# Performance work log

Measured on AMD Instinct MI355X. Metric: run time of the kernel, lower is better.

## Reference

```python
import jax, jax.numpy as jnp
import numpy as np

QUERY_DIM = 1024
KEY_DIM = 1024
NUM_HEADS = 16
HEAD_DIM = QUERY_DIM // NUM_HEADS


def setup_inputs() -> dict:
    key = jax.random.key(0)
    ks = jax.random.split(key, 11)
    B, Sq, Sk = 2, 2048, 2048
    s = 0.02
    return {
        "q": jax.random.normal(ks[0], (B, Sq, QUERY_DIM), jnp.float32),
        "k": jax.random.normal(ks[1], (B, Sk, KEY_DIM), jnp.float32),
        "v": jax.random.normal(ks[2], (B, Sk, KEY_DIM), jnp.float32),
        "Wq": jax.random.normal(ks[3], (QUERY_DIM, QUERY_DIM), jnp.float32) * s,
        "bq": jnp.zeros((QUERY_DIM,), jnp.float32),
        "Wk": jax.random.normal(ks[4], (KEY_DIM, QUERY_DIM), jnp.float32) * s,
        "bk": jnp.zeros((QUERY_DIM,), jnp.float32),
        "Wv": jax.random.normal(ks[5], (KEY_DIM, QUERY_DIM), jnp.float32) * s,
        "bv": jnp.zeros((QUERY_DIM,), jnp.float32),
        "Wo": jax.random.normal(ks[6], (QUERY_DIM, QUERY_DIM), jnp.float32) * s,
        "bo": jnp.zeros((QUERY_DIM,), jnp.float32),
    }


def reference(q, k, v, Wq, bq, Wk, bk, Wv, bv, Wo, bo):
    B, Sq, _ = q.shape
    Sk = k.shape[1]
    scale = HEAD_DIM ** -0.5
    # projections -> [B, H, S, Dh]
    qh = (q @ Wq + bq).reshape(B, Sq, NUM_HEADS, HEAD_DIM).transpose(0, 2, 1, 3)
    kh = (k @ Wk + bk).reshape(B, Sk, NUM_HEADS, HEAD_DIM).transpose(0, 2, 1, 3)
    vh = (v @ Wv + bv).reshape(B, Sk, NUM_HEADS, HEAD_DIM).transpose(0, 2, 1, 3)
    scores = jnp.einsum("bhqd,bhkd->bhqk", qh, kh) * scale
    attn = jax.nn.softmax(scores, axis=-1)
    out = jnp.einsum("bhqk,bhkd->bhqd", attn, vh)
    out = out.transpose(0, 2, 1, 3).reshape(B, Sq, QUERY_DIM)
    return out @ Wo + bo  # dropout is identity at inference
```

## Files before the change

### kernel.cpp

```cpp
#include <hip/hip_runtime.h>
#include <hip/hip_fp16.h>
#include <cstddef>


#define B_   2
#define S_   2048
#define D_   1024
#define H_   16
#define DH_  64

typedef _Float16 half8 __attribute__((ext_vector_type(8)));
typedef _Float16 half4 __attribute__((ext_vector_type(4)));
typedef float floatx4 __attribute__((ext_vector_type(4)));

#define MFMA32(a, b, c) __builtin_amdgcn_mfma_f32_16x16x32_f16((a), (b), (c), 0, 0, 0)
#define MFMA16(a, b, c) __builtin_amdgcn_mfma_f32_16x16x16f16((a), (b), (c), 0, 0, 0)

__global__ __launch_bounds__(256) void cvt3(
    const float* __restrict__ q, const float* __restrict__ k,
    const float* __restrict__ v,
    __half* __restrict__ qf, __half* __restrict__ kf, __half* __restrict__ vf)
{
    const float* srcs[3] = {q, k, v};
    __half* dsts[3] = {qf, kf, vf};
    const int z = blockIdx.y;
    const int i = blockIdx.x * 256 + threadIdx.x;
    const float4* s = (const float4*)srcs[z];
    const float4 a = s[2 * i], b = s[2 * i + 1];
    half8 h;
    h[0] = (_Float16)a.x; h[1] = (_Float16)a.y; h[2] = (_Float16)a.z; h[3] = (_Float16)a.w;
    h[4] = (_Float16)b.x; h[5] = (_Float16)b.y; h[6] = (_Float16)b.z; h[7] = (_Float16)b.w;
    *(half8*)&dsts[z][(size_t)i * 8] = h;
}

__global__ __launch_bounds__(256) void wtrans4(
    const float* __restrict__ Wq, const float* __restrict__ Wk,
    const float* __restrict__ Wv, const float* __restrict__ Wo,
    __half* __restrict__ Wtq, __half* __restrict__ Wtk,
    __half* __restrict__ Wtv, __half* __restrict__ Wto)
{
    __shared__ __align__(16) __half T[64][72];
    const float* Ws[4] = {Wq, Wk, Wv, Wo};
    __half* Wts[4] = {Wtq, Wtk, Wtv, Wto};
    const float* W = Ws[blockIdx.z];
    __half* Wt = Wts[blockIdx.z];
    const int tid = threadIdx.x;
    const int n0 = blockIdx.x * 64, k0 = blockIdx.y * 64;
    #pragma unroll
    for (int p = 0; p < 4; ++p) {
        const int c = tid + p * 256;
        const int kr = c >> 4, nc = (c & 15) * 4;
        const float4 a = *(const float4*)&W[(size_t)(k0 + kr) * D_ + n0 + nc];
        T[nc + 0][kr] = __float2half(a.x);
        T[nc + 1][kr] = __float2half(a.y);
        T[nc + 2][kr] = __float2half(a.z);
        T[nc + 3][kr] = __float2half(a.w);
    }
    __syncthreads();
    #pragma unroll
    for (int p = 0; p < 2; ++p) {
        const int c = tid + p * 256;
        const int nr = c >> 3, kc = (c & 7) * 8;
        *(half8*)&Wt[(size_t)(n0 + nr) * D_ + k0 + kc] = *(const half8*)&T[nr][kc];
    }
}

__device__ __forceinline__ void gemm_core(
    const __half* __restrict__ A, const __half* __restrict__ Bt,
    const float* __restrict__ bias, void* __restrict__ dst,
    const int mode, const float oscale)
{
    __shared__ __align__(16) char gsm[36864];
    __half (*As)[72] = (__half(*)[72])gsm;
    __half (*Bs)[72] = (__half(*)[72])(gsm + 18432);

    const int tid = threadIdx.x;
    const int m0 = blockIdx.y * 128, n0 = blockIdx.x * 128;
    const int lane = tid & 63, wv = tid >> 6;
    const int quad = lane >> 4, lr = lane & 15;
    const int wm0 = (wv >> 1) * 64, wn0 = (wv & 1) * 64;

    floatx4 acc[4][4];
    #pragma unroll
    for (int i = 0; i < 4; ++i)
        #pragma unroll
        for (int j = 0; j < 4; ++j)
            acc[i][j] = (floatx4){0.f, 0.f, 0.f, 0.f};

    half8 pa[4], pb[4];
    #pragma unroll
    for (int p = 0; p < 4; ++p) {
        const int c = tid + p * 256;
        const int row = c >> 3, seg = (c & 7) * 8;
        pa[p] = *(const half8*)&A [(size_t)(m0 + row) * D_ + seg];
        pb[p] = *(const half8*)&Bt[(size_t)(n0 + row) * D_ + seg];
    }

    for (int k0 = 0; k0 < D_; k0 += 64) {
        __syncthreads();
        #pragma unroll
        for (int p = 0; p < 4; ++p) {
            const int c = tid + p * 256;
            const int row = c >> 3, seg = (c & 7) * 8;
            *(half8*)&As[row][seg] = pa[p];
            *(half8*)&Bs[row][seg] = pb[p];
        }
        if (k0 + 64 < D_) {
            #pragma unroll
            for (int p = 0; p < 4; ++p) {
                const int c = tid + p * 256;
                const int row = c >> 3, seg = (c & 7) * 8;
                pa[p] = *(const half8*)&A [(size_t)(m0 + row) * D_ + k0 + 64 + seg];
                pb[p] = *(const half8*)&Bt[(size_t)(n0 + row) * D_ + k0 + 64 + seg];
            }
        }
        __syncthreads();
        #pragma unroll
        for (int ks = 0; ks < 2; ++ks) {
            const int ko = quad * 8 + ks * 32;
            half8 af[4], bf[4];
            #pragma unroll
            for (int i = 0; i < 4; ++i) af[i] = *(const half8*)&As[wm0 + i * 16 + lr][ko];
            #pragma unroll
            for (int j = 0; j < 4; ++j) bf[j] = *(const half8*)&Bs[wn0 + j * 16 + lr][ko];
            #pragma unroll
            for (int i = 0; i < 4; ++i)
                #pragma unroll
                for (int j = 0; j < 4; ++j)
                    acc[i][j] = MFMA32(af[i], bf[j], acc[i][j]);
        }
    }

    if (mode == 1) {
        float* out = (float*)dst;
        #pragma unroll
        for (int i = 0; i < 4; ++i) {
            #pragma unroll
            for (int j = 0; j < 4; ++j) {
                const int col = n0 + wn0 + j * 16 + lr;
                const float bval = bias[col];
                #pragma unroll
                for (int r = 0; r < 4; ++r) {
                    const int m = m0 + wm0 + i * 16 + quad * 4 + r;
                    out[(size_t)m * D_ + col] = acc[i][j][r] + bval;
                }
            }
        }
        return;
    }

    __syncthreads();
    __half (*Ct)[136] = (__half(*)[136])gsm;
    #pragma unroll
    for (int i = 0; i < 4; ++i) {
        #pragma unroll
        for (int j = 0; j < 4; ++j) {
            const int nl = wn0 + j * 16 + lr;
            const float bval = bias[n0 + nl];
            #pragma unroll
            for (int r = 0; r < 4; ++r) {
                const int ml = wm0 + i * 16 + quad * 4 + r;
                const _Float16 hv = (_Float16)((acc[i][j][r] + bval) * oscale);
                if (mode == 0) Ct[ml][nl] = hv;
                else           Ct[nl][ml] = hv;
            }
        }
    }
    __syncthreads();
    __half* oh = (__half*)dst;
    #pragma unroll
    for (int p = 0; p < 8; ++p) {
        const int row = (tid >> 4) + p * 16;
        const int cs  = (tid & 15) * 8;
        const half8 vls = *(const half8*)&Ct[row][cs];
        if (mode == 0) {
            const int m = m0 + row, col = n0 + cs;
            const int b = m >> 11, s = m & (S_ - 1);
            const int h = col >> 6, d = col & 63;
            *(half8*)&oh[(((size_t)(b * H_ + h) * S_ + s) << 6) + d] = vls;
        } else {
            const int col = n0 + row, m = m0 + cs;
            const int b = m >> 11, s = m & (S_ - 1);
            const int h = col >> 6, d = col & 63;
            *(half8*)&oh[((size_t)(b * H_ + h) * DH_ + d) * S_ + s] = vls;
        }
    }
}

__global__ __launch_bounds__(256) void gemm_proj(
    const __half* __restrict__ qf, const __half* __restrict__ kf,
    const __half* __restrict__ vf,
    const __half* __restrict__ Wtq, const __half* __restrict__ Wtk,
    const __half* __restrict__ Wtv,
    const float* __restrict__ bq, const float* __restrict__ bk,
    const float* __restrict__ bv,
    __half* __restrict__ qhf, __half* __restrict__ khf, __half* __restrict__ vht)
{
    const __half* As[3] = {qf, kf, vf};
    const __half* Bts[3] = {Wtq, Wtk, Wtv};
    const float* bs[3] = {bq, bk, bv};
    __half* ds[3] = {qhf, khf, vht};
    const int z = blockIdx.z;
    gemm_core(As[z], Bts[z], bs[z], ds[z], z == 2 ? 2 : 0,
              z == 0 ? 0.1803368801111244f : 1.0f);
}

__global__ __launch_bounds__(256) void gemm_final(
    const __half* __restrict__ attf, const __half* __restrict__ Wto,
    const float* __restrict__ bo, float* __restrict__ out)
{
    gemm_core(attf, Wto, bo, out, 1, 1.0f);
}

__global__ __launch_bounds__(256) void attn_f16(
    const __half* __restrict__ qhf, const __half* __restrict__ khf,
    const __half* __restrict__ vht, __half* __restrict__ attf)
{
    __shared__ __align__(16) char smem[31232];
    __half (*Qs)[72] = (__half(*)[72])smem;
    __half (*Ks)[72] = (__half(*)[72])(smem + 9216);
    __half (*Vs)[72] = (__half(*)[72])(smem + 18432);

    const int tid = threadIdx.x;
    const int lane = tid & 63, wv = tid >> 6;
    const int quad = lane >> 4, lr = lane & 15;
    const int bh = blockIdx.y;
    const int q0 = blockIdx.x * 64;
    const size_t hbase = (size_t)bh * S_ * DH_;

    #pragma unroll
    for (int p = 0; p < 2; ++p) {
        const int c = tid + p * 256;
        const int row = c >> 3, seg = (c & 7) * 8;
        *(half8*)&Qs[row][seg] = *(const half8*)&qhf[hbase + (size_t)(q0 + row) * DH_ + seg];
    }
    __syncthreads();
    half8 qB[4][2];
    #pragma unroll
    for (int qs = 0; qs < 4; ++qs)
        #pragma unroll
        for (int ks = 0; ks < 2; ++ks)
            qB[qs][ks] = *(const half8*)&Qs[qs * 16 + lr][quad * 8 + ks * 32];

    float lp[4] = {0.f, 0.f, 0.f, 0.f};
    floatx4 O[4][4];
    #pragma unroll
    for (int i = 0; i < 4; ++i)
        #pragma unroll
        for (int j = 0; j < 4; ++j)
            O[i][j] = (floatx4){0.f, 0.f, 0.f, 0.f};

    half8 pk[2], pv[2];
    #pragma unroll
    for (int p = 0; p < 2; ++p) {
        const int c = tid + p * 256;
        const int row = c >> 3, seg = (c & 7) * 8;
        pk[p] = *(const half8*)&khf[hbase + (size_t)row * DH_ + seg];
        pv[p] = *(const half8*)&vht[hbase + (size_t)row * S_ + seg];
    }

    for (int kt = 0; kt < S_; kt += 64) {
        __syncthreads();
        #pragma unroll
        for (int p = 0; p < 2; ++p) {
            const int c = tid + p * 256;
            const int row = c >> 3, seg = (c & 7) * 8;
            *(half8*)&Ks[row][seg] = pk[p];
            *(half8*)&Vs[row][seg] = pv[p];
        }
        if (kt + 64 < S_) {
            #pragma unroll
            for (int p = 0; p < 2; ++p) {
                const int c = tid + p * 256;
                const int row = c >> 3, seg = (c & 7) * 8;
                pk[p] = *(const half8*)&khf[hbase + (size_t)(kt + 64 + row) * DH_ + seg];
                pv[p] = *(const half8*)&vht[hbase + (size_t)row * S_ + kt + 64 + seg];
            }
        }
        __syncthreads();

        floatx4 s4[4];
        #pragma unroll
        for (int qs = 0; qs < 4; ++qs) s4[qs] = (floatx4){0.f, 0.f, 0.f, 0.f};
        #pragma unroll
        for (int ks = 0; ks < 2; ++ks) {
            const half8 aK = *(const half8*)&Ks[wv * 16 + lr][quad * 8 + ks * 32];
            #pragma unroll
            for (int qs = 0; qs < 4; ++qs)
                s4[qs] = MFMA32(aK, qB[qs][ks], s4[qs]);
        }

        half4 pB[4];
        #pragma unroll
        for (int qs = 0; qs < 4; ++qs) {
            #pragma unroll
            for (int r = 0; r < 4; ++r) {
                const float p = __builtin_amdgcn_exp2f(s4[qs][r]);
                lp[qs] += p;
                pB[qs][r] = (_Float16)p;
            }
        }

        #pragma unroll
        for (int ds = 0; ds < 4; ++ds) {
            const half4 aV = *(const half4*)&Vs[ds * 16 + lr][wv * 16 + quad * 4];
            #pragma unroll
            for (int qs = 0; qs < 4; ++qs)
                O[ds][qs] = MFMA16(aV, pB[qs], O[ds][qs]);
        }
    }

    __syncthreads();
    float* L    = (float*)(smem + 17408);
    float* invL = (float*)(smem + 21504);
    float (*R)[68] = (float(*)[68])smem;
    __half (*F)[72] = (__half(*)[72])(smem + 22016);

    #pragma unroll
    for (int qs = 0; qs < 4; ++qs)
        L[(wv * 4 + quad) * 64 + qs * 16 + lr] = lp[qs];
    __syncthreads();
    if (tid < 64) {
        float s = 0.f;
        #pragma unroll
        for (int i = 0; i < 16; ++i) s += L[i * 64 + tid];
        invL[tid] = 1.0f / s;
    }
    __syncthreads();

    const int qc = tid & 63, dg = tid >> 6;
    const float il = invL[qc];

    #pragma unroll
    for (int ds = 0; ds < 4; ++ds) {
        __syncthreads();
        #pragma unroll
        for (int qs = 0; qs < 4; ++qs)
            #pragma unroll
            for (int r = 0; r < 4; ++r)
                R[wv * 16 + quad * 4 + r][qs * 16 + lr] = O[ds][qs][r];
        __syncthreads();
        half4 hv;
        #pragma unroll
        for (int rr = 0; rr < 4; ++rr) {
            const int row = dg * 4 + rr;
            const float v = R[row][qc] + R[16 + row][qc] + R[32 + row][qc] + R[48 + row][qc];
            hv[rr] = (_Float16)(v * il);
        }
        *(half4*)&F[qc][ds * 16 + dg * 4] = hv;
    }
    __syncthreads();

    const int b = bh >> 4, h = bh & 15;
    const int qrow = tid >> 2, dseg = (tid & 3) * 16;
    __half* dstp = &attf[(((size_t)(b * S_ + q0 + qrow)) << 10) + h * DH_ + dseg];
    *(half8*)&dstp[0] = *(const half8*)&F[qrow][dseg];
    *(half8*)&dstp[8] = *(const half8*)&F[qrow][dseg + 8];
}

extern "C" void kernel_launch(void* const* d_in, const int* in_sizes, int n_in,
                              void* d_out, int out_size, void* d_ws, size_t ws_size,
                              hipStream_t stream) {
    const float* q  = (const float*)d_in[0];
    const float* k  = (const float*)d_in[1];
    const float* v  = (const float*)d_in[2];
    const float* Wq = (const float*)d_in[3];
    const float* bq = (const float*)d_in[4];
    const float* Wk = (const float*)d_in[5];
    const float* bk = (const float*)d_in[6];
    const float* Wv = (const float*)d_in[7];
    const float* bv = (const float*)d_in[8];
    const float* Wo = (const float*)d_in[9];
    const float* bo = (const float*)d_in[10];
    float* out = (float*)d_out;

    __half* ws = (__half*)d_ws;
    const size_t NE = (size_t)B_ * S_ * D_;
    __half* qf   = ws;
    __half* kf   = ws + NE;
    __half* vf   = ws + 2 * NE;
    __half* qhf  = ws + 3 * NE;
    __half* khf  = ws + 4 * NE;
    __half* vht  = ws + 5 * NE;
    __half* attf = ws + 6 * NE;
    __half* Wtq  = ws + 7 * NE;
    __half* Wtk  = Wtq + (size_t)D_ * D_;
    __half* Wtv  = Wtk + (size_t)D_ * D_;
    __half* Wto  = Wtv + (size_t)D_ * D_;

    const dim3 blk(256);
    cvt3<<<dim3((unsigned)(NE / 8 / 256), 3), blk, 0, stream>>>(q, k, v, qf, kf, vf);
    wtrans4<<<dim3(16, 16, 4), blk, 0, stream>>>(Wq, Wk, Wv, Wo, Wtq, Wtk, Wtv, Wto);

    gemm_proj<<<dim3(D_ / 128, (B_ * S_) / 128, 3), blk, 0, stream>>>(
        qf, kf, vf, Wtq, Wtk, Wtv, bq, bk, bv, qhf, khf, vht);

    attn_f16<<<dim3(S_ / 64, B_ * H_), blk, 0, stream>>>(qhf, khf, vht, attf);

    gemm_final<<<dim3(D_ / 128, (B_ * S_) / 128), blk, 0, stream>>>(attf, Wto, bo, out);
}
```

Measured before the change: 233.6 us.

## Widen attention key tile to 128, load Q directly to registers, set occupancy hint

```diff
diff --git a/kernel.cpp b/kernel.cpp
--- a/kernel.cpp
+++ b/kernel.cpp
@@ -212,14 +212,13 @@
     gemm_core(attf, Wto, bo, out, 1, 1.0f);
 }
 
-__global__ __launch_bounds__(256) void attn_f16(
+__global__ __launch_bounds__(256, 4) void attn_f16(
     const __half* __restrict__ qhf, const __half* __restrict__ khf,
     const __half* __restrict__ vht, __half* __restrict__ attf)
 {
-    __shared__ __align__(16) char smem[31232];
-    __half (*Qs)[72] = (__half(*)[72])smem;
-    __half (*Ks)[72] = (__half(*)[72])(smem + 9216);
-    __half (*Vs)[72] = (__half(*)[72])(smem + 18432);
+    __shared__ __align__(16) char smem[35840];
+    __half (*Ks)[72]  = (__half(*)[72])smem;
+    __half (*Vs)[136] = (__half(*)[136])(smem + 18432);
 
     const int tid = threadIdx.x;
     const int lane = tid & 63, wv = tid >> 6;
@@ -228,19 +227,13 @@
     const int q0 = blockIdx.x * 64;
     const size_t hbase = (size_t)bh * S_ * DH_;
 
-    #pragma unroll
-    for (int p = 0; p < 2; ++p) {
-        const int c = tid + p * 256;
-        const int row = c >> 3, seg = (c & 7) * 8;
-        *(half8*)&Qs[row][seg] = *(const half8*)&qhf[hbase + (size_t)(q0 + row) * DH_ + seg];
-    }
-    __syncthreads();
     half8 qB[4][2];
     #pragma unroll
     for (int qs = 0; qs < 4; ++qs)
         #pragma unroll
         for (int ks = 0; ks < 2; ++ks)
-            qB[qs][ks] = *(const half8*)&Qs[qs * 16 + lr][quad * 8 + ks * 32];
+            qB[qs][ks] = *(const half8*)&qhf[hbase
+                + (size_t)(q0 + qs * 16 + lr) * DH_ + quad * 8 + ks * 32];
 
     float lp[4] = {0.f, 0.f, 0.f, 0.f};
     floatx4 O[4][4];
@@ -250,63 +243,65 @@
         for (int j = 0; j < 4; ++j)
             O[i][j] = (floatx4){0.f, 0.f, 0.f, 0.f};
 
-    half8 pk[2], pv[2];
-    #pragma unroll
-    for (int p = 0; p < 2; ++p) {
+    half8 pk[4], pv[4];
+    #pragma unroll
+    for (int p = 0; p < 4; ++p) {
         const int c = tid + p * 256;
-        const int row = c >> 3, seg = (c & 7) * 8;
-        pk[p] = *(const half8*)&khf[hbase + (size_t)row * DH_ + seg];
-        pv[p] = *(const half8*)&vht[hbase + (size_t)row * S_ + seg];
-    }
-
-    for (int kt = 0; kt < S_; kt += 64) {
-        __syncthreads();
-        #pragma unroll
-        for (int p = 0; p < 2; ++p) {
+        pk[p] = *(const half8*)&khf[hbase + (size_t)(c >> 3) * DH_ + (c & 7) * 8];
+        pv[p] = *(const half8*)&vht[hbase + (size_t)(c >> 4) * S_ + (c & 15) * 8];
+    }
+
+    for (int kt = 0; kt < S_; kt += 128) {
+        __syncthreads();
+        #pragma unroll
+        for (int p = 0; p < 4; ++p) {
             const int c = tid + p * 256;
-            const int row = c >> 3, seg = (c & 7) * 8;
-            *(half8*)&Ks[row][seg] = pk[p];
-            *(half8*)&Vs[row][seg] = pv[p];
-        }
-        if (kt + 64 < S_) {
-            #pragma unroll
-            for (int p = 0; p < 2; ++p) {
+            *(half8*)&Ks[c >> 3][(c & 7) * 8] = pk[p];
+            *(half8*)&Vs[c >> 4][(c & 15) * 8] = pv[p];
+        }
+        if (kt + 128 < S_) {
+            #pragma unroll
+            for (int p = 0; p < 4; ++p) {
                 const int c = tid + p * 256;
-                const int row = c >> 3, seg = (c & 7) * 8;
-                pk[p] = *(const half8*)&khf[hbase + (size_t)(kt + 64 + row) * DH_ + seg];
-                pv[p] = *(const half8*)&vht[hbase + (size_t)row * S_ + kt + 64 + seg];
-            }
-        }
-        __syncthreads();
-
-        floatx4 s4[4];
-        #pragma unroll
-        for (int qs = 0; qs < 4; ++qs) s4[qs] = (floatx4){0.f, 0.f, 0.f, 0.f};
-        #pragma unroll
-        for (int ks = 0; ks < 2; ++ks) {
-            const half8 aK = *(const half8*)&Ks[wv * 16 + lr][quad * 8 + ks * 32];
-            #pragma unroll
-            for (int qs = 0; qs < 4; ++qs)
-                s4[qs] = MFMA32(aK, qB[qs][ks], s4[qs]);
-        }
-
-        half4 pB[4];
-        #pragma unroll
-        for (int qs = 0; qs < 4; ++qs) {
-            #pragma unroll
-            for (int r = 0; r < 4; ++r) {
-                const float p = __builtin_amdgcn_exp2f(s4[qs][r]);
-                lp[qs] += p;
-                pB[qs][r] = (_Float16)p;
-            }
-        }
-
-        #pragma unroll
-        for (int ds = 0; ds < 4; ++ds) {
-            const half4 aV = *(const half4*)&Vs[ds * 16 + lr][wv * 16 + quad * 4];
-            #pragma unroll
-            for (int qs = 0; qs < 4; ++qs)
-                O[ds][qs] = MFMA16(aV, pB[qs], O[ds][qs]);
+                pk[p] = *(const half8*)&khf[hbase
+                    + (size_t)(kt + 128 + (c >> 3)) * DH_ + (c & 7) * 8];
+                pv[p] = *(const half8*)&vht[hbase
+                    + (size_t)(c >> 4) * S_ + kt + 128 + (c & 15) * 8];
+            }
+        }
+        __syncthreads();
+
+        #pragma unroll
+        for (int h = 0; h < 2; ++h) {
+            floatx4 s4[4];
+            #pragma unroll
+            for (int qs = 0; qs < 4; ++qs) s4[qs] = (floatx4){0.f, 0.f, 0.f, 0.f};
+            #pragma unroll
+            for (int ks = 0; ks < 2; ++ks) {
+                const half8 aK = *(const half8*)&Ks[h * 64 + wv * 16 + lr][quad * 8 + ks * 32];
+                #pragma unroll
+                for (int qs = 0; qs < 4; ++qs)
+                    s4[qs] = MFMA32(aK, qB[qs][ks], s4[qs]);
+            }
+
+            half4 pB[4];
+            #pragma unroll
+            for (int qs = 0; qs < 4; ++qs) {
+                #pragma unroll
+                for (int r = 0; r < 4; ++r) {
+                    const float p = __builtin_amdgcn_exp2f(s4[qs][r]);
+                    lp[qs] += p;
+                    pB[qs][r] = (_Float16)p;
+                }
+            }
+
+            #pragma unroll
+            for (int ds = 0; ds < 4; ++ds) {
+                const half4 aV = *(const half4*)&Vs[ds * 16 + lr][h * 64 + wv * 16 + quad * 4];
+                #pragma unroll
+                for (int qs = 0; qs < 4; ++qs)
+                    O[ds][qs] = MFMA16(aV, pB[qs], O[ds][qs]);
+            }
         }
     }
 
```

New measurement: 732.8 us. +213.7%, slower.

## Split attention work by query rows per wave instead of key slices

Applied to the files above, without the earlier changes.

```diff
diff --git a/kernel.cpp b/kernel.cpp
--- a/kernel.cpp
+++ b/kernel.cpp
@@ -212,14 +212,13 @@
     gemm_core(attf, Wto, bo, out, 1, 1.0f);
 }
 
-__global__ __launch_bounds__(256) void attn_f16(
+__global__ __launch_bounds__(256, 4) void attn_f16(
     const __half* __restrict__ qhf, const __half* __restrict__ khf,
     const __half* __restrict__ vht, __half* __restrict__ attf)
 {
-    __shared__ __align__(16) char smem[31232];
-    __half (*Qs)[72] = (__half(*)[72])smem;
-    __half (*Ks)[72] = (__half(*)[72])(smem + 9216);
-    __half (*Vs)[72] = (__half(*)[72])(smem + 18432);
+    __shared__ __align__(16) char smem[18432];
+    __half (*Ks)[72] = (__half(*)[72])smem;
+    __half (*Vs)[72] = (__half(*)[72])(smem + 9216);
 
     const int tid = threadIdx.x;
     const int lane = tid & 63, wv = tid >> 6;
@@ -228,27 +227,16 @@
     const int q0 = blockIdx.x * 64;
     const size_t hbase = (size_t)bh * S_ * DH_;
 
-    #pragma unroll
-    for (int p = 0; p < 2; ++p) {
-        const int c = tid + p * 256;
-        const int row = c >> 3, seg = (c & 7) * 8;
-        *(half8*)&Qs[row][seg] = *(const half8*)&qhf[hbase + (size_t)(q0 + row) * DH_ + seg];
-    }
-    __syncthreads();
-    half8 qB[4][2];
-    #pragma unroll
-    for (int qs = 0; qs < 4; ++qs)
-        #pragma unroll
-        for (int ks = 0; ks < 2; ++ks)
-            qB[qs][ks] = *(const half8*)&Qs[qs * 16 + lr][quad * 8 + ks * 32];
-
-    float lp[4] = {0.f, 0.f, 0.f, 0.f};
-    floatx4 O[4][4];
-    #pragma unroll
-    for (int i = 0; i < 4; ++i)
-        #pragma unroll
-        for (int j = 0; j < 4; ++j)
-            O[i][j] = (floatx4){0.f, 0.f, 0.f, 0.f};
+    half8 qB[2];
+    #pragma unroll
+    for (int ks = 0; ks < 2; ++ks)
+        qB[ks] = *(const half8*)&qhf[hbase
+            + (size_t)(q0 + wv * 16 + lr) * DH_ + quad * 8 + ks * 32];
+
+    float lp = 0.f;
+    floatx4 O[4];
+    #pragma unroll
+    for (int i = 0; i < 4; ++i) O[i] = (floatx4){0.f, 0.f, 0.f, 0.f};
 
     half8 pk[2], pv[2];
     #pragma unroll
@@ -281,73 +269,49 @@
 
         floatx4 s4[4];
         #pragma unroll
-        for (int qs = 0; qs < 4; ++qs) s4[qs] = (floatx4){0.f, 0.f, 0.f, 0.f};
+        for (int ksub = 0; ksub < 4; ++ksub) s4[ksub] = (floatx4){0.f, 0.f, 0.f, 0.f};
         #pragma unroll
         for (int ks = 0; ks < 2; ++ks) {
-            const half8 aK = *(const half8*)&Ks[wv * 16 + lr][quad * 8 + ks * 32];
-            #pragma unroll
-            for (int qs = 0; qs < 4; ++qs)
-                s4[qs] = MFMA32(aK, qB[qs][ks], s4[qs]);
+            #pragma unroll
+            for (int ksub = 0; ksub < 4; ++ksub) {
+                const half8 aK = *(const half8*)&Ks[ksub * 16 + lr][quad * 8 + ks * 32];
+                s4[ksub] = MFMA32(aK, qB[ks], s4[ksub]);
+            }
         }
 
         half4 pB[4];
         #pragma unroll
-        for (int qs = 0; qs < 4; ++qs) {
+        for (int ksub = 0; ksub < 4; ++ksub) {
             #pragma unroll
             for (int r = 0; r < 4; ++r) {
-                const float p = __builtin_amdgcn_exp2f(s4[qs][r]);
-                lp[qs] += p;
-                pB[qs][r] = (_Float16)p;
+                const float p = __builtin_amdgcn_exp2f(s4[ksub][r]);
+                lp += p;
+                pB[ksub][r] = (_Float16)p;
             }
         }
 
         #pragma unroll
         for (int ds = 0; ds < 4; ++ds) {
-            const half4 aV = *(const half4*)&Vs[ds * 16 + lr][wv * 16 + quad * 4];
-            #pragma unroll
-            for (int qs = 0; qs < 4; ++qs)
-                O[ds][qs] = MFMA16(aV, pB[qs], O[ds][qs]);
-        }
-    }
-
-    __syncthreads();
-    float* L    = (float*)(smem + 17408);
-    float* invL = (float*)(smem + 21504);
-    float (*R)[68] = (float(*)[68])smem;
-    __half (*F)[72] = (__half(*)[72])(smem + 22016);
-
-    #pragma unroll
-    for (int qs = 0; qs < 4; ++qs)
-        L[(wv * 4 + quad) * 64 + qs * 16 + lr] = lp[qs];
-    __syncthreads();
-    if (tid < 64) {
-        float s = 0.f;
-        #pragma unroll
-        for (int i = 0; i < 16; ++i) s += L[i * 64 + tid];
-        invL[tid] = 1.0f / s;
-    }
-    __syncthreads();
-
-    const int qc = tid & 63, dg = tid >> 6;
-    const float il = invL[qc];
-
+            #pragma unroll
+            for (int ksl = 0; ksl < 4; ++ksl) {
+                const half4 aV = *(const half4*)&Vs[ds * 16 + lr][ksl * 16 + quad * 4];
+                O[ds] = MFMA16(aV, pB[ksl], O[ds]);
+            }
+        }
+    }
+
+    lp += __shfl_xor(lp, 16, 64);
+    lp += __shfl_xor(lp, 32, 64);
+    const float il = 1.0f / lp;
+
+    __syncthreads();
+    __half (*F)[72] = (__half(*)[72])smem;
     #pragma unroll
     for (int ds = 0; ds < 4; ++ds) {
-        __syncthreads();
-        #pragma unroll
-        for (int qs = 0; qs < 4; ++qs)
-            #pragma unroll
-            for (int r = 0; r < 4; ++r)
-                R[wv * 16 + quad * 4 + r][qs * 16 + lr] = O[ds][qs][r];
-        __syncthreads();
         half4 hv;
         #pragma unroll
-        for (int rr = 0; rr < 4; ++rr) {
-            const int row = dg * 4 + rr;
-            const float v = R[row][qc] + R[16 + row][qc] + R[32 + row][qc] + R[48 + row][qc];
-            hv[rr] = (_Float16)(v * il);
-        }
-        *(half4*)&F[qc][ds * 16 + dg * 4] = hv;
+        for (int r = 0; r < 4; ++r) hv[r] = (_Float16)(O[ds][r] * il);
+        *(half4*)&F[wv * 16 + lr][ds * 16 + quad * 4] = hv;
     }
     __syncthreads();
 
```

Measured after the change: 243.3 us. 1.04x slower.

## Double-buffer K/V tiles in attention and merge prep kernels into one launch

Applied to the files above, without the earlier changes.

```diff
diff --git a/kernel.cpp b/kernel.cpp
--- a/kernel.cpp
+++ b/kernel.cpp
@@ -16,52 +16,55 @@
 #define MFMA32(a, b, c) __builtin_amdgcn_mfma_f32_16x16x32_f16((a), (b), (c), 0, 0, 0)
 #define MFMA16(a, b, c) __builtin_amdgcn_mfma_f32_16x16x16f16((a), (b), (c), 0, 0, 0)
 
-__global__ __launch_bounds__(256) void cvt3(
+__global__ __launch_bounds__(256) void prep(
     const float* __restrict__ q, const float* __restrict__ k,
     const float* __restrict__ v,
-    __half* __restrict__ qf, __half* __restrict__ kf, __half* __restrict__ vf)
-{
-    const float* srcs[3] = {q, k, v};
-    __half* dsts[3] = {qf, kf, vf};
-    const int z = blockIdx.y;
-    const int i = blockIdx.x * 256 + threadIdx.x;
-    const float4* s = (const float4*)srcs[z];
-    const float4 a = s[2 * i], b = s[2 * i + 1];
-    half8 h;
-    h[0] = (_Float16)a.x; h[1] = (_Float16)a.y; h[2] = (_Float16)a.z; h[3] = (_Float16)a.w;
-    h[4] = (_Float16)b.x; h[5] = (_Float16)b.y; h[6] = (_Float16)b.z; h[7] = (_Float16)b.w;
-    *(half8*)&dsts[z][(size_t)i * 8] = h;
-}
-
-__global__ __launch_bounds__(256) void wtrans4(
+    __half* __restrict__ qf, __half* __restrict__ kf, __half* __restrict__ vf,
     const float* __restrict__ Wq, const float* __restrict__ Wk,
     const float* __restrict__ Wv, const float* __restrict__ Wo,
     __half* __restrict__ Wtq, __half* __restrict__ Wtk,
     __half* __restrict__ Wtv, __half* __restrict__ Wto)
 {
     __shared__ __align__(16) __half T[64][72];
+    const int tid = threadIdx.x;
+    const int z = blockIdx.z;
+    if (z < 3) {
+        const float* srcs[3] = {q, k, v};
+        __half* dsts[3] = {qf, kf, vf};
+        const int i = blockIdx.x * 256 + tid;
+        const float4* s = (const float4*)srcs[z];
+        const float4 a = s[2 * i], b = s[2 * i + 1];
+        half8 h;
+        h[0] = (_Float16)a.x; h[1] = (_Float16)a.y; h[2] = (_Float16)a.z; h[3] = (_Float16)a.w;
+        h[4] = (_Float16)b.x; h[5] = (_Float16)b.y; h[6] = (_Float16)b.z; h[7] = (_Float16)b.w;
+        *(half8*)&dsts[z][(size_t)i * 8] = h;
+        return;
+    }
+    if (blockIdx.x >= 256) return;
     const float* Ws[4] = {Wq, Wk, Wv, Wo};
     __half* Wts[4] = {Wtq, Wtk, Wtv, Wto};
-    const float* W = Ws[blockIdx.z];
-    __half* Wt = Wts[blockIdx.z];
-    const int tid = threadIdx.x;
-    const int n0 = blockIdx.x * 64, k0 = blockIdx.y * 64;
-    #pragma unroll
-    for (int p = 0; p < 4; ++p) {
-        const int c = tid + p * 256;
-        const int kr = c >> 4, nc = (c & 15) * 4;
-        const float4 a = *(const float4*)&W[(size_t)(k0 + kr) * D_ + n0 + nc];
-        T[nc + 0][kr] = __float2half(a.x);
-        T[nc + 1][kr] = __float2half(a.y);
-        T[nc + 2][kr] = __float2half(a.z);
-        T[nc + 3][kr] = __float2half(a.w);
-    }
-    __syncthreads();
-    #pragma unroll
-    for (int p = 0; p < 2; ++p) {
-        const int c = tid + p * 256;
-        const int nr = c >> 3, kc = (c & 7) * 8;
-        *(half8*)&Wt[(size_t)(n0 + nr) * D_ + k0 + kc] = *(const half8*)&T[nr][kc];
+    const int n0 = (blockIdx.x & 15) * 64, k0 = (blockIdx.x >> 4) * 64;
+    for (int w = 0; w < 4; ++w) {
+        const float* W = Ws[w];
+        __half* Wt = Wts[w];
+        #pragma unroll
+        for (int p = 0; p < 4; ++p) {
+            const int c = tid + p * 256;
+            const int kr = c >> 4, nc = (c & 15) * 4;
+            const float4 a = *(const float4*)&W[(size_t)(k0 + kr) * D_ + n0 + nc];
+            T[nc + 0][kr] = __float2half(a.x);
+            T[nc + 1][kr] = __float2half(a.y);
+            T[nc + 2][kr] = __float2half(a.z);
+            T[nc + 3][kr] = __float2half(a.w);
+        }
+        __syncthreads();
+        #pragma unroll
+        for (int p = 0; p < 2; ++p) {
+            const int c = tid + p * 256;
+            const int nr = c >> 3, kc = (c & 7) * 8;
+            *(half8*)&Wt[(size_t)(n0 + nr) * D_ + k0 + kc] = *(const half8*)&T[nr][kc];
+        }
+        __syncthreads();
     }
 }
 
@@ -216,10 +219,7 @@
     const __half* __restrict__ qhf, const __half* __restrict__ khf,
     const __half* __restrict__ vht, __half* __restrict__ attf)
 {
-    __shared__ __align__(16) char smem[31232];
-    __half (*Qs)[72] = (__half(*)[72])smem;
-    __half (*Ks)[72] = (__half(*)[72])(smem + 9216);
-    __half (*Vs)[72] = (__half(*)[72])(smem + 18432);
+    __shared__ __align__(16) char smem[36864];
 
     const int tid = threadIdx.x;
     const int lane = tid & 63, wv = tid >> 6;
@@ -228,60 +228,73 @@
     const int q0 = blockIdx.x * 64;
     const size_t hbase = (size_t)bh * S_ * DH_;
 
+    half8 qB[4][2];
+    #pragma unroll
+    for (int qs = 0; qs < 4; ++qs)
+        #pragma unroll
+        for (int ks = 0; ks < 2; ++ks)
+            qB[qs][ks] = *(const half8*)&qhf[hbase
+                + (size_t)(q0 + qs * 16 + lr) * DH_ + quad * 8 + ks * 32];
+
+    float lp[4] = {0.f, 0.f, 0.f, 0.f};
+    floatx4 O[4][4];
+    #pragma unroll
+    for (int i = 0; i < 4; ++i)
+        #pragma unroll
+        for (int j = 0; j < 4; ++j)
+            O[i][j] = (floatx4){0.f, 0.f, 0.f, 0.f};
+
+    {
+        __half (*K0)[72] = (__half(*)[72])smem;
+        __half (*V0)[72] = (__half(*)[72])(smem + 9216);
+        #pragma unroll
+        for (int p = 0; p < 2; ++p) {
+            const int c = tid + p * 256;
+            const int row = c >> 3, seg = (c & 7) * 8;
+            *(half8*)&K0[row][seg] = *(const half8*)&khf[hbase + (size_t)row * DH_ + seg];
+            *(half8*)&V0[row][seg] = *(const half8*)&vht[hbase + (size_t)row * S_ + seg];
+        }
+    }
+    half8 pk[2], pv[2];
     #pragma unroll
     for (int p = 0; p < 2; ++p) {
         const int c = tid + p * 256;
         const int row = c >> 3, seg = (c & 7) * 8;
-        *(half8*)&Qs[row][seg] = *(const half8*)&qhf[hbase + (size_t)(q0 + row) * DH_ + seg];
-    }
-    __syncthreads();
-    half8 qB[4][2];
-    #pragma unroll
-    for (int qs = 0; qs < 4; ++qs)
-        #pragma unroll
-        for (int ks = 0; ks < 2; ++ks)
-            qB[qs][ks] = *(const half8*)&Qs[qs * 16 + lr][quad * 8 + ks * 32];
-
-    float lp[4] = {0.f, 0.f, 0.f, 0.f};
-    floatx4 O[4][4];
-    #pragma unroll
-    for (int i = 0; i < 4; ++i)
-        #pragma unroll
-        for (int j = 0; j < 4; ++j)
-            O[i][j] = (floatx4){0.f, 0.f, 0.f, 0.f};
-
-    half8 pk[2], pv[2];
-    #pragma unroll
-    for (int p = 0; p < 2; ++p) {
-        const int c = tid + p * 256;
-        const int row = c >> 3, seg = (c & 7) * 8;
-        pk[p] = *(const half8*)&khf[hbase + (size_t)row * DH_ + seg];
-        pv[p] = *(const half8*)&vht[hbase + (size_t)row * S_ + seg];
-    }
+        pk[p] = *(const half8*)&khf[hbase + (size_t)(64 + row) * DH_ + seg];
+        pv[p] = *(const half8*)&vht[hbase + (size_t)row * S_ + 64 + seg];
+    }
+    __syncthreads();
 
     for (int kt = 0; kt < S_; kt += 64) {
-        __syncthreads();
-        #pragma unroll
-        for (int p = 0; p < 2; ++p) {
-            const int c = tid + p * 256;
-            const int row = c >> 3, seg = (c & 7) * 8;
-            *(half8*)&Ks[row][seg] = pk[p];
-            *(half8*)&Vs[row][seg] = pv[p];
-        }
+        const int cb = (kt >> 6) & 1;
+        __half (*Ks)[72] = (__half(*)[72])(smem + cb * 18432);
+        __half (*Vs)[72] = (__half(*)[72])(smem + cb * 18432 + 9216);
+        __half (*Kn)[72] = (__half(*)[72])(smem + (cb ^ 1) * 18432);
+        __half (*Vn)[72] = (__half(*)[72])(smem + (cb ^ 1) * 18432 + 9216);
+
         if (kt + 64 < S_) {
             #pragma unroll
             for (int p = 0; p < 2; ++p) {
                 const int c = tid + p * 256;
                 const int row = c >> 3, seg = (c & 7) * 8;
-                pk[p] = *(const half8*)&khf[hbase + (size_t)(kt + 64 + row) * DH_ + seg];
-                pv[p] = *(const half8*)&vht[hbase + (size_t)row * S_ + kt + 64 + seg];
-            }
-        }
-        __syncthreads();
+                *(half8*)&Kn[row][seg] = pk[p];
+                *(half8*)&Vn[row][seg] = pv[p];
+            }
+            if (kt + 128 < S_) {
+                #pragma unroll
+                for (int p = 0; p < 2; ++p) {
+                    const int c = tid + p * 256;
+                    const int row = c >> 3, seg = (c & 7) * 8;
+                    pk[p] = *(const half8*)&khf[hbase + (size_t)(kt + 128 + row) * DH_ + seg];
+                    pv[p] = *(const half8*)&vht[hbase + (size_t)row * S_ + kt + 128 + seg];
+                }
+            }
+        }
 
         floatx4 s4[4];
         #pragma unroll
         for (int qs = 0; qs < 4; ++qs) s4[qs] = (floatx4){0.f, 0.f, 0.f, 0.f};
+        __builtin_amdgcn_s_setprio(1);
         #pragma unroll
         for (int ks = 0; ks < 2; ++ks) {
             const half8 aK = *(const half8*)&Ks[wv * 16 + lr][quad * 8 + ks * 32];
@@ -289,6 +302,12 @@
             for (int qs = 0; qs < 4; ++qs)
                 s4[qs] = MFMA32(aK, qB[qs][ks], s4[qs]);
         }
+        __builtin_amdgcn_s_setprio(0);
+
+        half4 aV[4];
+        #pragma unroll
+        for (int ds = 0; ds < 4; ++ds)
+            aV[ds] = *(const half4*)&Vs[ds * 16 + lr][wv * 16 + quad * 4];
 
         half4 pB[4];
         #pragma unroll
@@ -301,16 +320,17 @@
             }
         }
 
-        #pragma unroll
-        for (int ds = 0; ds < 4; ++ds) {
-            const half4 aV = *(const half4*)&Vs[ds * 16 + lr][wv * 16 + quad * 4];
+        __builtin_amdgcn_s_setprio(1);
+        #pragma unroll
+        for (int ds = 0; ds < 4; ++ds)
             #pragma unroll
             for (int qs = 0; qs < 4; ++qs)
-                O[ds][qs] = MFMA16(aV, pB[qs], O[ds][qs]);
-        }
-    }
-
-    __syncthreads();
+                O[ds][qs] = MFMA16(aV[ds], pB[qs], O[ds][qs]);
+        __builtin_amdgcn_s_setprio(0);
+
+        __syncthreads();
+    }
+
     float* L    = (float*)(smem + 17408);
     float* invL = (float*)(smem + 21504);
     float (*R)[68] = (float(*)[68])smem;
@@ -389,8 +409,8 @@
     __half* Wto  = Wtv + (size_t)D_ * D_;
 
     const dim3 blk(256);
-    cvt3<<<dim3((unsigned)(NE / 8 / 256), 3), blk, 0, stream>>>(q, k, v, qf, kf, vf);
-    wtrans4<<<dim3(16, 16, 4), blk, 0, stream>>>(Wq, Wk, Wv, Wo, Wtq, Wtk, Wtv, Wto);
+    prep<<<dim3((unsigned)(NE / 8 / 256), 1, 4), blk, 0, stream>>>(
+        q, k, v, qf, kf, vf, Wq, Wk, Wv, Wo, Wtq, Wtk, Wtv, Wto);
 
     gemm_proj<<<dim3(D_ / 128, (B_ * S_) / 128, 3), blk, 0, stream>>>(
         qf, kf, vf, Wtq, Wtk, Wtv, bq, bk, bv, qhf, khf, vht);
```

Result: slower. 239.7 us (+2.6%).
